# Kernel tuning notes

Hardware: AMD Instinct MI355X
Metric: run time of the kernel (lower is better)

The kernel has to match this reference:

```python
import jax, jax.numpy as jnp
import numpy as np

K = 3          # kernel size
STRIDE = 1
PAD = 1
DIL = 1
BN_EPS = 1e-5


def _conv2d(x, w, b, stride=STRIDE, pad=PAD):
    out = jax.lax.conv_general_dilated(
        x, w, (stride, stride), [(pad, pad), (pad, pad)],
        dimension_numbers=("NCHW", "OIHW", "NCHW"))
    return out + b[None, :, None, None]


def _bilinear_sample(x, py, px):
    """Zero-padded bilinear sampling. x: [B,C,H,W]; py,px: [B,Ho,Wo] float coords."""
    B, C, H, W = x.shape
    y0 = jnp.floor(py)
    x0 = jnp.floor(px)
    wy1 = py - y0
    wx1 = px - x0
    x_flat = x.reshape(B, C, H * W)

    def gather(yi, xi, wgt):
        valid = (yi >= 0) & (yi <= H - 1) & (xi >= 0) & (xi <= W - 1)
        yc = jnp.clip(yi, 0, H - 1).astype(jnp.int32)
        xc = jnp.clip(xi, 0, W - 1).astype(jnp.int32)
        idx = (yc * W + xc).reshape(B, 1, -1)                      # [B,1,Ho*Wo]
        v = jnp.take_along_axis(x_flat, idx, axis=2)               # [B,C,Ho*Wo]
        v = v.reshape(B, C, py.shape[1], py.shape[2])
        return v * (wgt * valid)[:, None]

    return (gather(y0,     x0,     (1 - wy1) * (1 - wx1)) +
            gather(y0,     x0 + 1, (1 - wy1) * wx1) +
            gather(y0 + 1, x0,     wy1 * (1 - wx1)) +
            gather(y0 + 1, x0 + 1, wy1 * wx1))


def _forward(x, off_w, off_b, dc_w, dc_b, bn_gamma, bn_beta, bn_mean, bn_var):
    B, C, H, W = x.shape
    K2 = K * K
    om = _conv2d(x, off_w, off_b)                 # [B, 3*K2, H, W]
    offset = om[:, :2 * K2]                       # interleaved (dy, dx) per tap
    mask = jax.nn.sigmoid(om[:, 2 * K2:])         # [B, K2, H, W]

    # output pixel -> top-left input coordinate of the receptive field
    base_y = (jnp.arange(H) * STRIDE - PAD)[:, None]   # [H,1]
    base_x = (jnp.arange(W) * STRIDE - PAD)[None, :]   # [1,W]

    out = jnp.zeros((B, dc_w.shape[0], H, W), dtype=x.dtype)
    for k in range(K2):
        kh, kw = k // K, k % K
        py = base_y + kh * DIL + offset[:, 2 * k]      # [B,H,W]
        px = base_x + kw * DIL + offset[:, 2 * k + 1]  # [B,H,W]
        samp = _bilinear_sample(x, py, px) * mask[:, k][:, None]
        out = out + jnp.einsum('oc,bchw->bohw', dc_w[:, :, kh, kw], samp)
    out = out + dc_b[None, :, None, None]

    # BatchNorm (inference: running stats) + ReLU
    scale = bn_gamma / jnp.sqrt(bn_var + BN_EPS)
    out = out * scale[None, :, None, None] + (bn_beta - bn_mean * scale)[None, :, None, None]
    return jax.nn.relu(out)


def setup_inputs() -> dict:
    key = jax.random.key(0)
    ks = jax.random.split(key, 8)
    B, Cin, Cout, H, W = 8, 256, 256, 64, 64
    K2 = K * K
    x = jax.random.normal(ks[0], (B, Cin, H, W), dtype=jnp.float32)
    # NOTE: original init zeros the offset conv; we use small random weights so
    # offsets/masks are nontrivial and the bilinear path is exercised.
    off_w = jax.random.normal(ks[1], (3 * K2, Cin, K, K), dtype=jnp.float32) * 0.01
    off_b = jax.random.normal(ks[2], (3 * K2,), dtype=jnp.float32) * 0.01
    dc_w = jax.random.normal(ks[3], (Cout, Cin, K, K), dtype=jnp.float32) / np.sqrt(Cin * K2)
    dc_b = jax.random.normal(ks[4], (Cout,), dtype=jnp.float32) * 0.01
    bn_gamma = jnp.ones((Cout,), dtype=jnp.float32)
    bn_beta = jnp.zeros((Cout,), dtype=jnp.float32)
    bn_mean = jax.random.normal(ks[5], (Cout,), dtype=jnp.float32) * 0.1
    bn_var = jax.random.uniform(ks[6], (Cout,), dtype=jnp.float32) * 0.5 + 0.5
    return {"x": x, "off_w": off_w, "off_b": off_b, "dc_w": dc_w, "dc_b": dc_b,
            "bn_gamma": bn_gamma, "bn_beta": bn_beta,
            "bn_mean": bn_mean, "bn_var": bn_var}


def reference(x, off_w, off_b, dc_w, dc_b, bn_gamma, bn_beta, bn_mean, bn_var):
    return _forward(x, off_w, off_b, dc_w, dc_b, bn_gamma, bn_beta, bn_mean, bn_var)
```

## Files before the change

### kernel.cpp

```cpp
#include <hip/hip_runtime.h>
#include <hip/hip_bf16.h>
#include <hip/hip_fp16.h>
#include <cstdint>
#include <cstddef>

#define HH 64
#define WW 64
#define CIN 256
#define COUT 256
#define NB 8
#define HW (HH * WW)
#define BN_EPS 1e-5f

typedef __attribute__((ext_vector_type(8))) short s16x8;
typedef __attribute__((ext_vector_type(8))) unsigned short u16x8;
typedef __attribute__((ext_vector_type(4))) float f32x4;

static __device__ __forceinline__ float bf2f(unsigned short u) {
  unsigned int v = ((unsigned int)u) << 16;
  return __builtin_bit_cast(float, v);
}
static __device__ __forceinline__ unsigned short f2bf(float f) {
  __hip_bfloat16 h = __float2bfloat16(f);
  return __builtin_bit_cast(unsigned short, h);
}

__global__ __launch_bounds__(256) void k_tr(const float* __restrict__ x,
                                            unsigned short* __restrict__ xbf) {
  __shared__ float tile[64][65];
  int bid = blockIdx.x;
  int b = bid & 7;
  int r = bid >> 3;
  int ct = r & 3;
  int st = r >> 2;
  int lane = threadIdx.x & 63;
  int grp = threadIdx.x >> 6;
  int c0 = ct * 64, s0 = st * 64;
  const float* xb = x + (size_t)b * CIN * HW;
#pragma unroll
  for (int i = 0; i < 16; ++i) {
    int row = grp * 16 + i;
    tile[row][lane] = xb[(size_t)(c0 + row) * HW + s0 + lane];
  }
  __syncthreads();
  unsigned short* xo = xbf + (size_t)b * HW * CIN;
#pragma unroll
  for (int i = 0; i < 16; ++i) {
    int row = grp * 16 + i;
    xo[(size_t)(s0 + row) * CIN + c0 + lane] = f2bf(tile[lane][row]);
  }
}

__global__ __launch_bounds__(256) void k_wt(const float* __restrict__ dc_w,
                                            unsigned short* __restrict__ Wf) {
  int idx = blockIdx.x * 256 + threadIdx.x;
  if (idx >= 9 * 8 * 16 * 64 * 8) return;
  int j = idx & 7;
  int lane = (idx >> 3) & 63;
  int tile = (idx >> 9) & 15;
  int ks = (idx >> 13) & 7;
  int k = idx >> 16;
  int o = tile * 16 + (lane & 15);
  int c = ks * 32 + (lane >> 4) * 8 + j;
  Wf[idx] = f2bf(dc_w[((size_t)o * CIN + c) * 9 + k]);
}

__global__ __launch_bounds__(256) void k_owt(const float* __restrict__ off_w,
                                             unsigned short* __restrict__ OWf) {
  int idx = blockIdx.x * 256 + threadIdx.x;
  if (idx >= 9 * 8 * 2 * 64 * 8) return;
  int j = idx & 7;
  int lane = (idx >> 3) & 63;
  int kot = (idx >> 9) & 1;
  int ks = (idx >> 10) & 7;
  int t = idx >> 13;
  int ko = kot * 16 + (lane & 15);
  int c = ks * 32 + (lane >> 4) * 8 + j;
  unsigned short v = 0;
  if (ko < 27) v = f2bf(off_w[((size_t)ko * CIN + c) * 9 + t]);
  OWf[idx] = v;
}

__global__ void k_bn(const float* __restrict__ g, const float* __restrict__ be,
                     const float* __restrict__ m, const float* __restrict__ va,
                     const float* __restrict__ db, float* __restrict__ sc,
                     float* __restrict__ bi) {
  int o = threadIdx.x;
  float s = g[o] * rsqrtf(va[o] + BN_EPS);
  sc[o] = s;
  bi[o] = be[o] + (db[o] - m[o]) * s;
}

__global__ __launch_bounds__(256, 3) void k_main(
    const unsigned short* __restrict__ xbf, const unsigned short* __restrict__ OWf,
    const float* __restrict__ off_b, const unsigned short* __restrict__ Wf,
    const float* __restrict__ bnsc, const float* __restrict__ bnbi,
    float* __restrict__ out) {
  int bid = blockIdx.x;
  int b = bid & 7;
  int h = bid >> 3;
  int tid = threadIdx.x;
  int lane = tid & 63;
  int wave = tid >> 6;
  int l15 = lane & 15, l4 = lane >> 4;

  __shared__ __align__(16) unsigned short ubuf[66 * 256];
  __shared__ float om_lds[27][64];
  __shared__ unsigned short pre_offS[9][64][4];
  __shared__ __half pre_wH[9][64][4];

  const unsigned short* xb = xbf + (size_t)b * HW * CIN;

  if (tid < 64) {
    int r = (tid < 32) ? 0 : 65;
    int ch = tid & 31;
    u16x8 z = {0, 0, 0, 0, 0, 0, 0, 0};
    *(u16x8*)&ubuf[r * 256 + ch * 8] = z;
  }

  f32x4 acc_oc[2];
  acc_oc[0] = (f32x4){0.f, 0.f, 0.f, 0.f};
  acc_oc[1] = (f32x4){0.f, 0.f, 0.f, 0.f};
  int wavepx = wave * 16;

  for (int kh = 0; kh < 3; ++kh) {
    int y = h + kh - 1;
    if (y < 0 || y >= HH) continue;
    __syncthreads();
    const unsigned short* src = xb + (size_t)y * WW * CIN;
#pragma unroll
    for (int i = 0; i < 8; ++i) {
      int e8 = i * 256 + tid;
      int px = e8 >> 5;
      int ch = e8 & 31;
      u16x8 v = *(const u16x8*)(src + e8 * 8);
      *(u16x8*)&ubuf[(px + 1) * 256 + ((ch ^ ((px + 1) & 7)) * 8)] = v;
    }
    __syncthreads();
#pragma unroll
    for (int kw = 0; kw < 3; ++kw) {
      int prow = wavepx + l15 + kw;
      int rs = prow & 7;
      const unsigned short* Atap = OWf + ((size_t)(kh * 3 + kw) * 8) * 1024 + lane * 8;
#pragma unroll
      for (int ks = 0; ks < 8; ++ks) {
        s16x8 bfrag = *(const s16x8*)&ubuf[prow * 256 + (((ks * 4 + l4) ^ rs) * 8)];
#pragma unroll
        for (int kot = 0; kot < 2; ++kot) {
          s16x8 afrag = *(const s16x8*)(Atap + ks * 1024 + kot * 512);
          acc_oc[kot] = __builtin_amdgcn_mfma_f32_16x16x32_bf16(afrag, bfrag,
                                                                acc_oc[kot], 0, 0, 0);
        }
      }
    }
  }
#pragma unroll
  for (int kot = 0; kot < 2; ++kot) {
#pragma unroll
    for (int j = 0; j < 4; ++j) {
      int ko = kot * 16 + l4 * 4 + j;
      if (ko < 27) om_lds[ko][wavepx + l15] = acc_oc[kot][j];
    }
  }
  __syncthreads();

  for (int item = tid; item < 9 * 64; item += 256) {
    int k = item >> 6;
    int w = item & 63;
    int kh = k / 3, kw = k % 3;
    float offy = om_lds[2 * k][w] + off_b[2 * k];
    float offx = om_lds[2 * k + 1][w] + off_b[2 * k + 1];
    float mk = om_lds[18 + k][w] + off_b[18 + k];
    mk = 1.0f / (1.0f + expf(-mk));
    float py = (float)(h - 1 + kh) + offy;
    float px = (float)(w - 1 + kw) + offx;
    float fy0 = floorf(py), fx0 = floorf(px);
    float wy1 = py - fy0, wx1 = px - fx0;
    int y0 = (int)fy0, x0 = (int)fx0;
    int y1 = y0 + 1, x1 = x0 + 1;
    bool vy0 = (y0 >= 0) && (y0 <= HH - 1);
    bool vy1 = (y1 >= 0) && (y1 <= HH - 1);
    bool vx0 = (x0 >= 0) && (x0 <= WW - 1);
    bool vx1 = (x1 >= 0) && (x1 <= WW - 1);
    int y0c = min(max(y0, 0), HH - 1), y1c = min(max(y1, 0), HH - 1);
    int x0c = min(max(x0, 0), WW - 1), x1c = min(max(x1, 0), WW - 1);
    pre_wH[k][w][0] =
        __float2half((1.f - wy1) * (1.f - wx1) * mk * ((vy0 && vx0) ? 1.f : 0.f));
    pre_wH[k][w][1] = __float2half((1.f - wy1) * wx1 * mk * ((vy0 && vx1) ? 1.f : 0.f));
    pre_wH[k][w][2] = __float2half(wy1 * (1.f - wx1) * mk * ((vy1 && vx0) ? 1.f : 0.f));
    pre_wH[k][w][3] = __float2half(wy1 * wx1 * mk * ((vy1 && vx1) ? 1.f : 0.f));
    pre_offS[k][w][0] = (unsigned short)(y0c * WW + x0c);
    pre_offS[k][w][1] = (unsigned short)(y0c * WW + x1c);
    pre_offS[k][w][2] = (unsigned short)(y1c * WW + x0c);
    pre_offS[k][w][3] = (unsigned short)(y1c * WW + x1c);
  }

  unsigned short(*S)[256] = (unsigned short(*)[256])ubuf;
  f32x4 acc[4][4];
#pragma unroll
  for (int i = 0; i < 4; ++i)
#pragma unroll
    for (int j = 0; j < 4; ++j) acc[i][j] = (f32x4){0.f, 0.f, 0.f, 0.f};

  int pswz = lane & 7;
  int o_base = wave * 64;
  int hv = lane >> 5;
  int chunk = lane & 31;

  for (int k = 0; k < 9; ++k) {
    __syncthreads();
    {
#pragma unroll
      for (int pp = 0; pp < 8; ++pp) {
        int px = wavepx + pp * 2 + hv;
        int i0 = ((int)pre_offS[k][px][0]) << 8;
        int i1 = ((int)pre_offS[k][px][1]) << 8;
        int i2 = ((int)pre_offS[k][px][2]) << 8;
        int i3 = ((int)pre_offS[k][px][3]) << 8;
        float w0 = __half2float(pre_wH[k][px][0]);
        float w1 = __half2float(pre_wH[k][px][1]);
        float w2 = __half2float(pre_wH[k][px][2]);
        float w3 = __half2float(pre_wH[k][px][3]);
        u16x8 v0 = *(const u16x8*)(xb + i0 + chunk * 8);
        u16x8 v1 = *(const u16x8*)(xb + i1 + chunk * 8);
        u16x8 v2 = *(const u16x8*)(xb + i2 + chunk * 8);
        u16x8 v3 = *(const u16x8*)(xb + i3 + chunk * 8);
        u16x8 r;
#pragma unroll
        for (int j = 0; j < 8; ++j) {
          float s = w0 * bf2f(v0[j]) + w1 * bf2f(v1[j]) + w2 * bf2f(v2[j]) +
                    w3 * bf2f(v3[j]);
          r[j] = f2bf(s);
        }
        int phys = chunk ^ (px & 7);
        *(u16x8*)&S[px][phys * 8] = r;
      }
    }
    __syncthreads();
    const unsigned short* Wa = Wf + (size_t)k * 65536 + (wave * 4) * 512 + lane * 8;
#pragma unroll
    for (int ks = 0; ks < 8; ++ks) {
      s16x8 a[4], bf[4];
#pragma unroll
      for (int ot = 0; ot < 4; ++ot)
        a[ot] = *(const s16x8*)(Wa + ks * 8192 + ot * 512);
#pragma unroll
      for (int pt = 0; pt < 4; ++pt) {
        int slot = (ks * 4 + l4) ^ pswz;
        bf[pt] = *(const s16x8*)&S[pt * 16 + l15][slot * 8];
      }
#pragma unroll
      for (int ot = 0; ot < 4; ++ot)
#pragma unroll
        for (int pt = 0; pt < 4; ++pt)
          acc[ot][pt] = __builtin_amdgcn_mfma_f32_16x16x32_bf16(a[ot], bf[pt],
                                                                acc[ot][pt], 0, 0, 0);
    }
  }

#pragma unroll
  for (int ot = 0; ot < 4; ++ot) {
#pragma unroll
    for (int j = 0; j < 4; ++j) {
      int o = o_base + ot * 16 + l4 * 4 + j;
      float sc = bnsc[o], bi = bnbi[o];
      float* ob = out + (((size_t)b * COUT + o) * HH + h) * WW;
#pragma unroll
      for (int pt = 0; pt < 4; ++pt) {
        ob[pt * 16 + l15] = fmaxf(fmaf(acc[ot][pt][j], sc, bi), 0.f);
      }
    }
  }
}

extern "C" void kernel_launch(void* const* d_in, const int* in_sizes, int n_in,
                              void* d_out, int out_size, void* d_ws, size_t ws_size,
                              hipStream_t stream) {
  const float* x = (const float*)d_in[0];
  const float* off_w = (const float*)d_in[1];
  const float* off_b = (const float*)d_in[2];
  const float* dc_w = (const float*)d_in[3];
  const float* dc_b = (const float*)d_in[4];
  const float* bn_gamma = (const float*)d_in[5];
  const float* bn_beta = (const float*)d_in[6];
  const float* bn_mean = (const float*)d_in[7];
  const float* bn_var = (const float*)d_in[8];
  float* out = (float*)d_out;

  char* ws = (char*)d_ws;
  unsigned short* xbf = (unsigned short*)ws;
  ws += (size_t)NB * HW * CIN * sizeof(unsigned short);
  unsigned short* Wf = (unsigned short*)ws;
  ws += (size_t)9 * 8 * 16 * 64 * 8 * sizeof(unsigned short);
  unsigned short* OWf = (unsigned short*)ws;
  ws += (size_t)9 * 8 * 2 * 64 * 8 * sizeof(unsigned short);
  float* bnsc = (float*)ws;
  ws += 256 * sizeof(float);
  float* bnbi = (float*)ws;

  k_tr<<<NB * 64 * 4, 256, 0, stream>>>(x, xbf);
  k_wt<<<(9 * 8 * 16 * 64 * 8 + 255) / 256, 256, 0, stream>>>(dc_w, Wf);
  k_owt<<<(9 * 8 * 2 * 64 * 8 + 255) / 256, 256, 0, stream>>>(off_w, OWf);
  k_bn<<<1, 256, 0, stream>>>(bn_gamma, bn_beta, bn_mean, bn_var, dc_b, bnsc, bnbi);
  k_main<<<NB * HH, 256, 0, stream>>>(xbf, OWf, off_b, Wf, bnsc, bnbi, out);
}
```

Baseline: 107.4 us.

## Split each output row into two half-row blocks to double grid size

The main kernel now assigns half an output row (32 pixels) per block instead of a full row, doubling the grid and halving LDS and accumulator usage, so occupancy can rise to 4 blocks per CU. The input row staging now loads only a 34-column halo window with explicit zero padding. In exchange, the offset-conv phase runs on only two of the four waves, and the dc weights are streamed twice as often per output, raising weight traffic and the load-to-MFMA ratio.

```diff
diff --git a/kernel.cpp b/kernel.cpp
--- a/kernel.cpp
+++ b/kernel.cpp
@@ -91,86 +91,89 @@
   bi[o] = be[o] + (db[o] - m[o]) * s;
 }
 
-__global__ __launch_bounds__(256, 3) void k_main(
+__global__ __launch_bounds__(256, 4) void k_main(
     const unsigned short* __restrict__ xbf, const unsigned short* __restrict__ OWf,
     const float* __restrict__ off_b, const unsigned short* __restrict__ Wf,
     const float* __restrict__ bnsc, const float* __restrict__ bnbi,
     float* __restrict__ out) {
   int bid = blockIdx.x;
   int b = bid & 7;
-  int h = bid >> 3;
+  int r = bid >> 3;
+  int h = r & 63;
+  int q = r >> 6;
+  int wq = q * 32;
   int tid = threadIdx.x;
   int lane = tid & 63;
   int wave = tid >> 6;
   int l15 = lane & 15, l4 = lane >> 4;
 
-  __shared__ __align__(16) unsigned short ubuf[66 * 256];
-  __shared__ float om_lds[27][64];
-  __shared__ unsigned short pre_offS[9][64][4];
-  __shared__ __half pre_wH[9][64][4];
+  __shared__ __align__(16) unsigned short ubuf[34 * 256];
+  __shared__ float om_lds[27][32];
+  __shared__ unsigned short pre_offS[9][32][4];
+  __shared__ __half pre_wH[9][32][4];
 
   const unsigned short* xb = xbf + (size_t)b * HW * CIN;
-
-  if (tid < 64) {
-    int r = (tid < 32) ? 0 : 65;
-    int ch = tid & 31;
-    u16x8 z = {0, 0, 0, 0, 0, 0, 0, 0};
-    *(u16x8*)&ubuf[r * 256 + ch * 8] = z;
-  }
 
   f32x4 acc_oc[2];
   acc_oc[0] = (f32x4){0.f, 0.f, 0.f, 0.f};
   acc_oc[1] = (f32x4){0.f, 0.f, 0.f, 0.f};
-  int wavepx = wave * 16;
+  int ptile = wave & 1;
+  int gstart = wq - 1;
 
   for (int kh = 0; kh < 3; ++kh) {
     int y = h + kh - 1;
     if (y < 0 || y >= HH) continue;
     __syncthreads();
-    const unsigned short* src = xb + (size_t)y * WW * CIN;
-#pragma unroll
-    for (int i = 0; i < 8; ++i) {
-      int e8 = i * 256 + tid;
-      int px = e8 >> 5;
-      int ch = e8 & 31;
-      u16x8 v = *(const u16x8*)(src + e8 * 8);
-      *(u16x8*)&ubuf[(px + 1) * 256 + ((ch ^ ((px + 1) & 7)) * 8)] = v;
+    const unsigned short* srow = xb + (size_t)y * WW * CIN;
+    for (int e = tid; e < 34 * 32; e += 256) {
+      int col = e >> 5;
+      int ch = e & 31;
+      int g = gstart + col;
+      u16x8 v = {0, 0, 0, 0, 0, 0, 0, 0};
+      if (g >= 0 && g < WW) v = *(const u16x8*)(srow + (size_t)g * CIN + ch * 8);
+      *(u16x8*)&ubuf[col * 256 + ((ch ^ (col & 7)) * 8)] = v;
     }
     __syncthreads();
-#pragma unroll
-    for (int kw = 0; kw < 3; ++kw) {
-      int prow = wavepx + l15 + kw;
-      int rs = prow & 7;
-      const unsigned short* Atap = OWf + ((size_t)(kh * 3 + kw) * 8) * 1024 + lane * 8;
-#pragma unroll
-      for (int ks = 0; ks < 8; ++ks) {
-        s16x8 bfrag = *(const s16x8*)&ubuf[prow * 256 + (((ks * 4 + l4) ^ rs) * 8)];
-#pragma unroll
-        for (int kot = 0; kot < 2; ++kot) {
-          s16x8 afrag = *(const s16x8*)(Atap + ks * 1024 + kot * 512);
-          acc_oc[kot] = __builtin_amdgcn_mfma_f32_16x16x32_bf16(afrag, bfrag,
-                                                                acc_oc[kot], 0, 0, 0);
+    if (wave < 2) {
+#pragma unroll
+      for (int kw = 0; kw < 3; ++kw) {
+        int prow = ptile * 16 + l15 + kw;
+        int rs = prow & 7;
+        const unsigned short* Atap =
+            OWf + ((size_t)(kh * 3 + kw) * 8) * 1024 + lane * 8;
+#pragma unroll
+        for (int ks = 0; ks < 8; ++ks) {
+          s16x8 bfrag = *(const s16x8*)&ubuf[prow * 256 + (((ks * 4 + l4) ^ rs) * 8)];
+#pragma unroll
+          for (int kot = 0; kot < 2; ++kot) {
+            s16x8 afrag = *(const s16x8*)(Atap + ks * 1024 + kot * 512);
+            acc_oc[kot] = __builtin_amdgcn_mfma_f32_16x16x32_bf16(afrag, bfrag,
+                                                                  acc_oc[kot], 0, 0, 0);
+          }
         }
       }
     }
   }
-#pragma unroll
-  for (int kot = 0; kot < 2; ++kot) {
-#pragma unroll
-    for (int j = 0; j < 4; ++j) {
-      int ko = kot * 16 + l4 * 4 + j;
-      if (ko < 27) om_lds[ko][wavepx + l15] = acc_oc[kot][j];
+  if (wave < 2) {
+#pragma unroll
+    for (int kot = 0; kot < 2; ++kot) {
+#pragma unroll
+      for (int j = 0; j < 4; ++j) {
+        int ko = kot * 16 + l4 * 4 + j;
+        if (ko < 27) om_lds[ko][ptile * 16 + l15] = acc_oc[kot][j];
+      }
     }
   }
   __syncthreads();
 
-  for (int item = tid; item < 9 * 64; item += 256) {
-    int k = item >> 6;
-    int w = item & 63;
+  for (int item = tid; item < 9 * 32; item += 256) {
+    int k = item >> 5;
+    int wl = item & 31;
+    int w = wq + wl;
     int kh = k / 3, kw = k % 3;
-    float offy = om_lds[2 * k][w] + off_b[2 * k];
-    float offx = om_lds[2 * k + 1][w] + off_b[2 * k + 1];
-    float mk = om_lds[18 + k][w] + off_b[18 + k];
+    float offy = om_lds[2 * k][wl] + off_b[2 * k];
+    float offx = om_lds[2 * k + 1][wl] + off_b[2 * k + 1];
+    float mk = om_lds[18 + k][wl] + off_b[18 + k];
     mk = 1.0f / (1.0f + expf(-mk));
     float py = (float)(h - 1 + kh) + offy;
     float px = (float)(w - 1 + kw) + offx;
@@ -184,25 +187,24 @@
     bool vx1 = (x1 >= 0) && (x1 <= WW - 1);
     int y0c = min(max(y0, 0), HH - 1), y1c = min(max(y1, 0), HH - 1);
     int x0c = min(max(x0, 0), WW - 1), x1c = min(max(x1, 0), WW - 1);
-    pre_wH[k][w][0] =
+    pre_wH[k][wl][0] =
         __float2half((1.f - wy1) * (1.f - wx1) * mk * ((vy0 && vx0) ? 1.f : 0.f));
-    pre_wH[k][w][1] = __float2half((1.f - wy1) * wx1 * mk * ((vy0 && vx1) ? 1.f : 0.f));
-    pre_wH[k][w][2] = __float2half(wy1 * (1.f - wx1) * mk * ((vy1 && vx0) ? 1.f : 0.f));
-    pre_wH[k][w][3] = __float2half(wy1 * wx1 * mk * ((vy1 && vx1) ? 1.f : 0.f));
-    pre_offS[k][w][0] = (unsigned short)(y0c * WW + x0c);
-    pre_offS[k][w][1] = (unsigned short)(y0c * WW + x1c);
-    pre_offS[k][w][2] = (unsigned short)(y1c * WW + x0c);
-    pre_offS[k][w][3] = (unsigned short)(y1c * WW + x1c);
+    pre_wH[k][wl][1] = __float2half((1.f - wy1) * wx1 * mk * ((vy0 && vx1) ? 1.f : 0.f));
+    pre_wH[k][wl][2] = __float2half(wy1 * (1.f - wx1) * mk * ((vy1 && vx0) ? 1.f : 0.f));
+    pre_wH[k][wl][3] = __float2half(wy1 * wx1 * mk * ((vy1 && vx1) ? 1.f : 0.f));
+    pre_offS[k][wl][0] = (unsigned short)(y0c * WW + x0c);
+    pre_offS[k][wl][1] = (unsigned short)(y0c * WW + x1c);
+    pre_offS[k][wl][2] = (unsigned short)(y1c * WW + x0c);
+    pre_offS[k][wl][3] = (unsigned short)(y1c * WW + x1c);
   }
 
   unsigned short(*S)[256] = (unsigned short(*)[256])ubuf;
-  f32x4 acc[4][4];
+  f32x4 acc[4][2];
 #pragma unroll
   for (int i = 0; i < 4; ++i)
 #pragma unroll
-    for (int j = 0; j < 4; ++j) acc[i][j] = (f32x4){0.f, 0.f, 0.f, 0.f};
-
-  int pswz = lane & 7;
+    for (int j = 0; j < 2; ++j) acc[i][j] = (f32x4){0.f, 0.f, 0.f, 0.f};
+
   int o_base = wave * 64;
   int hv = lane >> 5;
   int chunk = lane & 31;
@@ -211,48 +213,49 @@
     __syncthreads();
     {
 #pragma unroll
-      for (int pp = 0; pp < 8; ++pp) {
-        int px = wavepx + pp * 2 + hv;
-        int i0 = ((int)pre_offS[k][px][0]) << 8;
-        int i1 = ((int)pre_offS[k][px][1]) << 8;
-        int i2 = ((int)pre_offS[k][px][2]) << 8;
-        int i3 = ((int)pre_offS[k][px][3]) << 8;
-        float w0 = __half2float(pre_wH[k][px][0]);
-        float w1 = __half2float(pre_wH[k][px][1]);
-        float w2 = __half2float(pre_wH[k][px][2]);
-        float w3 = __half2float(pre_wH[k][px][3]);
+      for (int pp = 0; pp < 4; ++pp) {
+        int pl = wave * 8 + pp * 2 + hv;
+        int i0 = ((int)pre_offS[k][pl][0]) << 8;
+        int i1 = ((int)pre_offS[k][pl][1]) << 8;
+        int i2 = ((int)pre_offS[k][pl][2]) << 8;
+        int i3 = ((int)pre_offS[k][pl][3]) << 8;
+        float w0 = __half2float(pre_wH[k][pl][0]);
+        float w1 = __half2float(pre_wH[k][pl][1]);
+        float w2 = __half2float(pre_wH[k][pl][2]);
+        float w3 = __half2float(pre_wH[k][pl][3]);
         u16x8 v0 = *(const u16x8*)(xb + i0 + chunk * 8);
         u16x8 v1 = *(const u16x8*)(xb + i1 + chunk * 8);
         u16x8 v2 = *(const u16x8*)(xb + i2 + chunk * 8);
         u16x8 v3 = *(const u16x8*)(xb + i3 + chunk * 8);
-        u16x8 r;
+        u16x8 rr;
 #pragma unroll
         for (int j = 0; j < 8; ++j) {
           float s = w0 * bf2f(v0[j]) + w1 * bf2f(v1[j]) + w2 * bf2f(v2[j]) +
                     w3 * bf2f(v3[j]);
-          r[j] = f2bf(s);
+          rr[j] = f2bf(s);
         }
-        int phys = chunk ^ (px & 7);
-        *(u16x8*)&S[px][phys * 8] = r;
+        int phys = chunk ^ (pl & 7);
+        *(u16x8*)&S[pl][phys * 8] = rr;
       }
     }
     __syncthreads();
     const unsigned short* Wa = Wf + (size_t)k * 65536 + (wave * 4) * 512 + lane * 8;
 #pragma unroll
     for (int ks = 0; ks < 8; ++ks) {
-      s16x8 a[4], bf[4];
+      s16x8 a[4], bf[2];
 #pragma unroll
       for (int ot = 0; ot < 4; ++ot)
         a[ot] = *(const s16x8*)(Wa + ks * 8192 + ot * 512);
 #pragma unroll
-      for (int pt = 0; pt < 4; ++pt) {
-        int slot = (ks * 4 + l4) ^ pswz;
-        bf[pt] = *(const s16x8*)&S[pt * 16 + l15][slot * 8];
+      for (int pt = 0; pt < 2; ++pt) {
+        int pl = pt * 16 + l15;
+        int slot = (ks * 4 + l4) ^ (pl & 7);
+        bf[pt] = *(const s16x8*)&S[pl][slot * 8];
       }
 #pragma unroll
       for (int ot = 0; ot < 4; ++ot)
 #pragma unroll
-        for (int pt = 0; pt < 4; ++pt)
+        for (int pt = 0; pt < 2; ++pt)
           acc[ot][pt] = __builtin_amdgcn_mfma_f32_16x16x32_bf16(a[ot], bf[pt],
                                                                 acc[ot][pt], 0, 0, 0);
     }
@@ -264,9 +267,9 @@
     for (int j = 0; j < 4; ++j) {
       int o = o_base + ot * 16 + l4 * 4 + j;
       float sc = bnsc[o], bi = bnbi[o];
-      float* ob = out + (((size_t)b * COUT + o) * HH + h) * WW;
-#pragma unroll
-      for (int pt = 0; pt < 4; ++pt) {
+      float* ob = out + (((size_t)b * COUT + o) * HH + h) * WW + wq;
+#pragma unroll
+      for (int pt = 0; pt < 2; ++pt) {
         ob[pt * 16 + l15] = fmaxf(fmaf(acc[ot][pt][j], sc, bi), 0.f);
       }
     }
@@ -302,5 +305,5 @@
   k_wt<<<(9 * 8 * 16 * 64 * 8 + 255) / 256, 256, 0, stream>>>(dc_w, Wf);
   k_owt<<<(9 * 8 * 2 * 64 * 8 + 255) / 256, 256, 0, stream>>>(off_w, OWf);
   k_bn<<<1, 256, 0, stream>>>(bn_gamma, bn_beta, bn_mean, bn_var, dc_b, bnsc, bnbi);
-  k_main<<<NB * HH, 256, 0, stream>>>(xbf, OWf, off_b, Wf, bnsc, bnbi, out);
-}
+  k_main<<<NB * HH * 2, 256, 0, stream>>>(xbf, OWf, off_b, Wf, bnsc, bnbi, out);
+}
```

Result: no change. 106.2 us (median of 2 runs) (-1.2%).
